# Performance work log

Hardware: AMD Instinct MI355X
Metric: run time of the kernel (lower is better)

The kernel has to match this reference:

```python
import jax, jax.numpy as jnp
import numpy as np

B, S, D = 1, 2048, 6144
H, KV, HD = 48, 8, 128  # query heads, kv heads, head dim
THETA = 10000.0


def _rope_tables(seq_len, head_dim, theta):
    pos = jnp.arange(seq_len, dtype=jnp.float32)
    inv_freq = 1.0 / (theta ** (jnp.arange(0, head_dim, 2, dtype=jnp.float32) / head_dim))
    freqs = pos[:, None] * inv_freq[None, :]                 # [S, HD/2]
    emb = jnp.concatenate([freqs, freqs], axis=-1)           # [S, HD]
    return jnp.cos(emb), jnp.sin(emb)


def setup_inputs() -> dict:
    key = jax.random.key(0)
    k1, k2, k3 = jax.random.split(key, 3)
    hidden_states = jax.random.normal(k1, (B, S, D), dtype=jnp.float32) * 0.02
    w_qkv = jax.random.normal(k2, (D, (H + 2 * KV) * HD), dtype=jnp.float32) * 0.02
    w_out = jax.random.normal(k3, (H * HD, D), dtype=jnp.float32) * 0.02
    cos, sin = _rope_tables(S, HD, THETA)
    return {"hidden_states": hidden_states, "cos": cos, "sin": sin,
            "w_qkv": w_qkv, "w_out": w_out}


def _rotate_half(x):
    x1, x2 = jnp.split(x, 2, axis=-1)
    return jnp.concatenate([-x2, x1], axis=-1)


def reference(hidden_states, cos, sin, w_qkv, w_out):
    b, s, d = hidden_states.shape
    # fused QKV projection
    qkv = jnp.einsum('bsd,de->bse', hidden_states, w_qkv)
    q = qkv[..., : H * HD].reshape(b, s, H, HD)
    k = qkv[..., H * HD: (H + KV) * HD].reshape(b, s, KV, HD)
    v = qkv[..., (H + KV) * HD:].reshape(b, s, KV, HD)
    # rotary embedding (rotate-half form)
    c = cos[None, :, None, :]
    sn = sin[None, :, None, :]
    q = q * c + _rotate_half(q) * sn
    k = k * c + _rotate_half(k) * sn
    # GQA: expand kv heads to query heads
    rep = H // KV
    k = jnp.repeat(k, rep, axis=2)  # [b, s, H, HD]
    v = jnp.repeat(v, rep, axis=2)
    scale = 1.0 / jnp.sqrt(jnp.float32(HD))
    scores = jnp.einsum('bqhd,bkhd->bhqk', q, k) * scale     # [b,H,S,S]
    causal = jnp.tril(jnp.ones((s, s), dtype=bool))
    scores = jnp.where(causal[None, None], scores, jnp.float32(-1e30))
    attn = jax.nn.softmax(scores, axis=-1)
    out = jnp.einsum('bhqk,bkhd->bqhd', attn, v).reshape(b, s, H * HD)
    return jnp.einsum('bsd,de->bse', out, w_out)
```

## Files before the change

kernel.cpp:

```cpp
#include <hip/hip_runtime.h>


#define S_   2048
#define D_   6144
#define H_   48
#define KV_  8
#define HD_  128
#define NQK  8192
#define REP  6

typedef __attribute__((ext_vector_type(8)))  __bf16 bf16x8;
typedef __attribute__((ext_vector_type(4)))  __bf16 bf16x4;
typedef __attribute__((ext_vector_type(2)))  __bf16 bf16x2;
typedef __attribute__((ext_vector_type(4)))  float  f32x4;
typedef __attribute__((ext_vector_type(16))) float  f32x16;
typedef __attribute__((ext_vector_type(4)))  float  float4v;

__device__ __forceinline__ void gl_lds16(const void* g, void* l) {
  __builtin_amdgcn_global_load_lds(
      (const __attribute__((address_space(1))) void*)g,
      (__attribute__((address_space(3))) void*)l, 16, 0, 0);
}

__device__ __forceinline__ unsigned pack2(float a, float b) {
  union { bf16x2 v; unsigned u; } x;
  x.v[0] = (__bf16)a; x.v[1] = (__bf16)b;
  return x.u;
}

__global__ __launch_bounds__(256) void cvt_bf16(const float* __restrict__ in,
                                                __bf16* __restrict__ out, int n4) {
  int stride = gridDim.x * 256;
  for (int i = blockIdx.x * 256 + threadIdx.x; i < n4; i += stride) {
    float4v v = ((const float4v*)in)[i];
    bf16x4 o;
    o[0] = (__bf16)v[0]; o[1] = (__bf16)v[1];
    o[2] = (__bf16)v[2]; o[3] = (__bf16)v[3];
    ((bf16x4*)out)[i] = o;
  }
}

__global__ __launch_bounds__(256) void wtrans(const float* __restrict__ src,
                                              __bf16* __restrict__ dst,
                                              int K, int N) {
  __shared__ float t[32][33];
  const int n0 = blockIdx.x * 32, k0 = blockIdx.y * 32;
  const int tx = threadIdx.x, ty = threadIdx.y;
#pragma unroll
  for (int r = 0; r < 4; ++r)
    t[ty + r * 8][tx] = src[(size_t)(k0 + ty + r * 8) * N + n0 + tx];
  __syncthreads();
#pragma unroll
  for (int r = 0; r < 4; ++r)
    dst[(size_t)(n0 + ty + r * 8) * K + k0 + tx] = (__bf16)t[tx][ty + r * 8];
}

__global__ __launch_bounds__(512, 2) void gemm_bt(const __bf16* __restrict__ A,
                                                  const __bf16* __restrict__ BT,
                                                  float* __restrict__ C,
                                                  int M, int N, int K) {
  __shared__ __align__(16) __bf16 As[2][256 * 64];
  __shared__ __align__(16) __bf16 Bs[2][256 * 64];
  const int tid = threadIdx.x;
  const int w = tid >> 6, l = tid & 63;
  const int lr = l & 15, lg = l >> 4;
  const int wm = w >> 2, wn = w & 3;
  const int nwg = gridDim.x * gridDim.y;
  int bid = blockIdx.y * gridDim.x + blockIdx.x;
  bid = (bid & 7) * (nwg >> 3) + (bid >> 3);
  const int m0 = (bid / gridDim.x) * 256, n0 = (bid % gridDim.x) * 256;
  const int nkt = K >> 6;

  auto stage_unit = [&](int T, int u) {
    const int buf = T & 1;
    const int k0 = T << 6;
    const __bf16* src = (u < 2) ? A : BT;
    const int base0 = (u < 2) ? m0 : n0;
    __bf16* dst = (u < 2) ? As[buf] : Bs[buf];
#pragma unroll
    for (int jj = 0; jj < 2; ++jj) {
      int j = (u & 1) * 2 + jj;
      int idx = j * 512 + tid;
      int row = idx >> 3;
      int c = (idx & 7) ^ (row & 7);
      gl_lds16(src + (size_t)(base0 + row) * K + k0 + c * 8,
               dst + (size_t)(j * 512 + w * 64) * 8);
    }
  };

  f32x4 acc[8][4] = {};
#pragma unroll
  for (int u = 0; u < 4; ++u) stage_unit(0, u);
  asm volatile("s_waitcnt vmcnt(0)" ::: "memory");
  __builtin_amdgcn_s_barrier();

  for (int T = 0; T < nkt; ++T) {
    const __bf16* Ab = As[T & 1];
    const __bf16* Bb = Bs[T & 1];
    bf16x8 bfr[4];
#pragma unroll
    for (int p = 0; p < 4; ++p) {
      const int kk = p >> 1, mh = p & 1;
      bf16x8 afr[4];
#pragma unroll
      for (int m = 0; m < 4; ++m) {
        int row = wm * 128 + (mh * 4 + m) * 16 + lr;
        afr[m] = *(const bf16x8*)(Ab + (size_t)row * 64
                                  + (((kk * 4 + lg) ^ (lr & 7)) * 8));
      }
      if (mh == 0) {
#pragma unroll
        for (int n = 0; n < 4; ++n) {
          int row = wn * 64 + n * 16 + lr;
          bfr[n] = *(const bf16x8*)(Bb + (size_t)row * 64
                                    + (((kk * 4 + lg) ^ (lr & 7)) * 8));
        }
      }
      if (p == 0 && T + 1 < nkt) {
#pragma unroll
        for (int u = 0; u < 4; ++u) stage_unit(T + 1, u);
      }
      if (p == 3 && T + 1 < nkt)
        asm volatile("s_waitcnt vmcnt(0)" ::: "memory");
      __builtin_amdgcn_s_barrier();
      asm volatile("s_waitcnt lgkmcnt(0)" ::: "memory");
      __builtin_amdgcn_sched_barrier(0);
      __builtin_amdgcn_s_setprio(1);
#pragma unroll
      for (int m = 0; m < 4; ++m)
#pragma unroll
        for (int n = 0; n < 4; ++n)
          acc[mh * 4 + m][n] = __builtin_amdgcn_mfma_f32_16x16x32_bf16(
              afr[m], bfr[n], acc[mh * 4 + m][n], 0, 0, 0);
      __builtin_amdgcn_s_setprio(0);
      __builtin_amdgcn_sched_barrier(0);
      __builtin_amdgcn_s_barrier();
    }
  }
#pragma unroll
  for (int m = 0; m < 8; ++m)
#pragma unroll
    for (int n = 0; n < 4; ++n)
#pragma unroll
      for (int j = 0; j < 4; ++j) {
        int row = m0 + wm * 128 + m * 16 + lg * 4 + j;
        int col = n0 + wn * 64 + n * 16 + lr;
        C[(size_t)row * N + col] = acc[m][n][j];
      }
}

__global__ __launch_bounds__(256) void rope_qk(const float* __restrict__ qkv,
                                               const float* __restrict__ cosT,
                                               const float* __restrict__ sinT,
                                               __bf16* __restrict__ Qo,
                                               __bf16* __restrict__ Ko) {
  const int s = blockIdx.x;
  const float* base = qkv + (size_t)s * NQK;
  const float* ct = cosT + s * HD_;
  const float* st = sinT + s * HD_;
  const float scale = 0.1275174313f;
  for (int idx = threadIdx.x; idx < H_ * HD_; idx += 256) {
    int h = idx >> 7, d = idx & 127;
    float x = base[idx];
    float r = (d < 64) ? -base[idx + 64] : base[idx - 64];
    Qo[((size_t)s * H_ + h) * HD_ + d] = (__bf16)((x * ct[d] + r * st[d]) * scale);
  }
  for (int idx = threadIdx.x; idx < KV_ * HD_; idx += 256) {
    int h = idx >> 7, d = idx & 127;
    float x = base[H_ * HD_ + idx];
    float r = (d < 64) ? -base[H_ * HD_ + idx + 64] : base[H_ * HD_ + idx - 64];
    Ko[((size_t)s * KV_ + h) * HD_ + d] = (__bf16)(x * ct[d] + r * st[d]);
  }
}

__global__ __launch_bounds__(256) void v_trans(const float* __restrict__ qkv,
                                               __bf16* __restrict__ Vt) {
  __shared__ float t[32][33];
  const int s0 = blockIdx.x * 32, d0 = blockIdx.y * 32, h = blockIdx.z;
  const int tx = threadIdx.x, ty = threadIdx.y;
#pragma unroll
  for (int r = 0; r < 4; ++r)
    t[ty + r * 8][tx] = qkv[(size_t)(s0 + ty + r * 8) * NQK + (H_ + KV_) * HD_ + h * HD_ + d0 + tx];
  __syncthreads();
#pragma unroll
  for (int r = 0; r < 4; ++r)
    Vt[((size_t)h * HD_ + d0 + ty + r * 8) * S_ + s0 + tx] = (__bf16)t[tx][ty + r * 8];
}

__global__ __launch_bounds__(256, 2) void attn(const __bf16* __restrict__ Q,
                                               const __bf16* __restrict__ Kb,
                                               const __bf16* __restrict__ Vt,
                                               __bf16* __restrict__ O) {
  __shared__ __align__(16) __bf16 Ks[2][64 * 128];
  __shared__ __align__(16) __bf16 Vs[2][128 * 64];
  const int bx = blockIdx.x, h = blockIdx.y, kvh = h / REP;
  const int tid = threadIdx.x, w = tid >> 6, l = tid & 63;
  const int c = l & 31, g = l >> 5;
  const int qb = bx * 128;
  const int qrow = qb + w * 32 + c;
  const int tmax_w = (qb + w * 32 + 31) >> 6;
  const int NT = (qb >> 6) + 2;

  auto stage = [&](int t) {
    const int buf = t & 1;
    const int kbase = t << 6;
#pragma unroll
    for (int j = 0; j < 4; ++j) {
      int idx = j * 256 + tid;
      int row = idx >> 4, cc = (idx & 15) ^ (row & 15);
      gl_lds16(Kb + ((size_t)(kbase + row) * KV_ + kvh) * HD_ + cc * 8,
               Ks[buf] + (size_t)(j * 256 + w * 64) * 8);
    }
#pragma unroll
    for (int j = 0; j < 4; ++j) {
      int idx = j * 256 + tid;
      int row = idx >> 3, cc = (idx & 7) ^ (row & 7);
      gl_lds16(Vt + (size_t)(kvh * HD_ + row) * S_ + kbase + cc * 8,
               Vs[buf] + (size_t)(j * 256 + w * 64) * 8);
    }
  };

  bf16x8 qf[8];
  const __bf16* qp = Q + ((size_t)qrow * H_ + h) * HD_ + g * 8;
#pragma unroll
  for (int st = 0; st < 8; ++st) qf[st] = *(const bf16x8*)(qp + st * 16);

  f32x16 o[4] = {};
  float m = -1e30f, lsum = 0.f;

  stage(0);
  __syncthreads();
  for (int t = 0; t < NT; ++t) {
    const int buf = t & 1;
    if (t + 1 < NT) stage(t + 1);
    if (t <= tmax_w) {
      const int kbase = t << 6;
      f32x16 s0 = {}, s1 = {};
      __builtin_amdgcn_s_setprio(1);
#pragma unroll
      for (int st = 0; st < 8; ++st) {
        int ch = ((st * 2 + g) ^ (c & 15)) * 8;
        bf16x8 k0 = *(const bf16x8*)(Ks[buf] + (size_t)c * 128 + ch);
        bf16x8 k1 = *(const bf16x8*)(Ks[buf] + (size_t)(32 + c) * 128 + ch);
        s0 = __builtin_amdgcn_mfma_f32_32x32x16_bf16(k0, qf[st], s0, 0, 0, 0);
        s1 = __builtin_amdgcn_mfma_f32_32x32x16_bf16(k1, qf[st], s1, 0, 0, 0);
      }
      __builtin_amdgcn_s_setprio(0);
      if (t == tmax_w) {
#pragma unroll
        for (int r = 0; r < 16; ++r) {
          int krow = (r & 3) + 8 * (r >> 2) + 4 * g;
          if (kbase + krow > qrow)      s0[r] = -1e30f;
          if (kbase + 32 + krow > qrow) s1[r] = -1e30f;
        }
      }
      float mj = s0[0];
#pragma unroll
      for (int r = 1; r < 16; ++r) mj = fmaxf(mj, s0[r]);
#pragma unroll
      for (int r = 0; r < 16; ++r) mj = fmaxf(mj, s1[r]);
      mj = fmaxf(mj, __shfl_xor(mj, 32));
      float mnew = fmaxf(m, mj);
      float sc = __builtin_amdgcn_exp2f(m - mnew);
      float rs = 0.f;
      float p0[16], p1[16];
#pragma unroll
      for (int r = 0; r < 16; ++r) { p0[r] = __builtin_amdgcn_exp2f(s0[r] - mnew); rs += p0[r]; }
#pragma unroll
      for (int r = 0; r < 16; ++r) { p1[r] = __builtin_amdgcn_exp2f(s1[r] - mnew); rs += p1[r]; }
      rs += __shfl_xor(rs, 32);
      lsum = lsum * sc + rs;
      m = mnew;
#pragma unroll
      for (int db = 0; db < 4; ++db)
#pragma unroll
        for (int r = 0; r < 16; ++r) o[db][r] *= sc;
      unsigned bq[4][4];
#pragma unroll
      for (int n = 0; n < 2; ++n)
#pragma unroll
        for (int tq = 0; tq < 2; ++tq) {
          const float* pp = n ? p1 : p0;
          unsigned q0 = pack2(pp[8 * tq + 0], pp[8 * tq + 1]);
          unsigned q1 = pack2(pp[8 * tq + 2], pp[8 * tq + 3]);
          unsigned q2 = pack2(pp[8 * tq + 4], pp[8 * tq + 5]);
          unsigned q3 = pack2(pp[8 * tq + 6], pp[8 * tq + 7]);
          unsigned v0 = g ? q0 : q2;
          unsigned v1 = g ? q1 : q3;
          unsigned sh0 = (unsigned)__shfl_xor((int)v0, 32);
          unsigned sh1 = (unsigned)__shfl_xor((int)v1, 32);
          int s = n * 2 + tq;
          bq[s][0] = g ? sh0 : q0;
          bq[s][1] = g ? sh1 : q1;
          bq[s][2] = g ? q2 : sh0;
          bq[s][3] = g ? q3 : sh1;
        }
      __builtin_amdgcn_s_setprio(1);
#pragma unroll
      for (int s = 0; s < 4; ++s) {
        union { unsigned u[4]; bf16x8 v; } bb;
        bb.u[0] = bq[s][0]; bb.u[1] = bq[s][1]; bb.u[2] = bq[s][2]; bb.u[3] = bq[s][3];
#pragma unroll
        for (int db = 0; db < 4; ++db) {
          int ch = ((s * 2 + g) ^ (c & 7)) * 8;
          bf16x8 vfr = *(const bf16x8*)(Vs[buf] + (size_t)(db * 32 + c) * 64 + ch);
          o[db] = __builtin_amdgcn_mfma_f32_32x32x16_bf16(vfr, bb.v, o[db], 0, 0, 0);
        }
      }
      __builtin_amdgcn_s_setprio(0);
    }
    if (t + 1 < NT) __syncthreads();
  }
  float inv = 1.f / lsum;
#pragma unroll
  for (int db = 0; db < 4; ++db)
#pragma unroll
    for (int rg = 0; rg < 4; ++rg) {
      bf16x4 ov;
#pragma unroll
      for (int j = 0; j < 4; ++j) ov[j] = (__bf16)(o[db][rg * 4 + j] * inv);
      *(bf16x4*)(O + (size_t)qrow * D_ + h * HD_ + db * 32 + rg * 8 + g * 4) = ov;
    }
}

extern "C" void kernel_launch(void* const* d_in, const int* in_sizes, int n_in,
                              void* d_out, int out_size, void* d_ws, size_t ws_size,
                              hipStream_t stream) {
  const float* hidden = (const float*)d_in[0];
  const float* cosT   = (const float*)d_in[1];
  const float* sinT   = (const float*)d_in[2];
  const float* w_qkv  = (const float*)d_in[3];
  const float* w_out  = (const float*)d_in[4];
  float* out = (float*)d_out;
  char* ws = (char*)d_ws;

  __bf16* wT  = (__bf16*)ws;
  __bf16* hb  = (__bf16*)(ws + 100663296);
  float*  qkv = (float*)(ws + 100663296 + 25165824);
  __bf16* q_b = (__bf16*)(ws + 100663296 + 25165824 + 67108864);
  __bf16* k_b = q_b + (size_t)S_ * H_ * HD_;
  __bf16* vt_b = k_b + (size_t)S_ * KV_ * HD_;

  cvt_bf16<<<dim3(2048), dim3(256), 0, stream>>>(hidden, hb, (int)((size_t)S_ * D_ / 4));
  wtrans<<<dim3(NQK / 32, D_ / 32), dim3(32, 8), 0, stream>>>(w_qkv, wT, D_, NQK);
  gemm_bt<<<dim3(NQK / 256, S_ / 256), dim3(512), 0, stream>>>(hb, wT, qkv, S_, NQK, D_);
  rope_qk<<<dim3(S_), dim3(256), 0, stream>>>(qkv, cosT, sinT, q_b, k_b);
  v_trans<<<dim3(S_ / 32, HD_ / 32, KV_), dim3(32, 8), 0, stream>>>(qkv, vt_b);
  wtrans<<<dim3(D_ / 32, D_ / 32), dim3(32, 8), 0, stream>>>(w_out, wT, D_, D_);
  attn<<<dim3(S_ / 128, H_), dim3(256), 0, stream>>>(q_b, k_b, vt_b, hb);
  gemm_bt<<<dim3(D_ / 256, S_ / 256), dim3(512), 0, stream>>>(hb, wT, out, S_, D_, D_);
}
```

Before: 713.0 us.

## Deepen GEMM LDS pipeline to four K=32 stages with three tiles in flight

Halves the GEMM K-tile from 64 to 32 and uses four LDS buffers, prefetching three tiles ahead instead of one. The vmcnt waits are changed from a full drain to partial waits, so global-to-LDS loads overlap more of the MFMA work. A new XOR swizzle suited to 32-wide rows is meant to avoid LDS bank conflicts. In exchange there are twice as many barriers per unit of K, and the waitcnt bookkeeping near the loop tail is more fragile.

```diff
diff --git a/kernel.cpp b/kernel.cpp
--- a/kernel.cpp
+++ b/kernel.cpp
@@ -59,8 +59,8 @@
                                                   const __bf16* __restrict__ BT,
                                                   float* __restrict__ C,
                                                   int M, int N, int K) {
-  __shared__ __align__(16) __bf16 As[2][256 * 64];
-  __shared__ __align__(16) __bf16 Bs[2][256 * 64];
+  __shared__ __align__(16) __bf16 As[4][256 * 32];
+  __shared__ __align__(16) __bf16 Bs[4][256 * 32];
   const int tid = threadIdx.x;
   const int w = tid >> 6, l = tid & 63;
   const int lr = l & 15, lg = l >> 4;
@@ -69,59 +69,52 @@
   int bid = blockIdx.y * gridDim.x + blockIdx.x;
   bid = (bid & 7) * (nwg >> 3) + (bid >> 3);
   const int m0 = (bid / gridDim.x) * 256, n0 = (bid % gridDim.x) * 256;
-  const int nkt = K >> 6;
-
-  auto stage_unit = [&](int T, int u) {
-    const int buf = T & 1;
-    const int k0 = T << 6;
-    const __bf16* src = (u < 2) ? A : BT;
-    const int base0 = (u < 2) ? m0 : n0;
-    __bf16* dst = (u < 2) ? As[buf] : Bs[buf];
-#pragma unroll
-    for (int jj = 0; jj < 2; ++jj) {
-      int j = (u & 1) * 2 + jj;
+  const int nkt = K >> 5;
+
+  auto stage = [&](int T) {
+    const int buf = T & 3;
+    const int k0 = T << 5;
+#pragma unroll
+    for (int j = 0; j < 2; ++j) {
       int idx = j * 512 + tid;
-      int row = idx >> 3;
-      int c = (idx & 7) ^ (row & 7);
-      gl_lds16(src + (size_t)(base0 + row) * K + k0 + c * 8,
-               dst + (size_t)(j * 512 + w * 64) * 8);
+      int row = idx >> 2;
+      int c = (idx & 3) ^ ((row ^ (row >> 2)) & 3);
+      gl_lds16(A  + (size_t)(m0 + row) * K + k0 + c * 8, As[buf] + (size_t)idx * 8);
+      gl_lds16(BT + (size_t)(n0 + row) * K + k0 + c * 8, Bs[buf] + (size_t)idx * 8);
     }
   };
 
   f32x4 acc[8][4] = {};
-#pragma unroll
-  for (int u = 0; u < 4; ++u) stage_unit(0, u);
-  asm volatile("s_waitcnt vmcnt(0)" ::: "memory");
+  stage(0); stage(1); stage(2);
+  asm volatile("s_waitcnt vmcnt(8)" ::: "memory");
   __builtin_amdgcn_s_barrier();
 
   for (int T = 0; T < nkt; ++T) {
-    const __bf16* Ab = As[T & 1];
-    const __bf16* Bb = Bs[T & 1];
+    const __bf16* Ab = As[T & 3];
+    const __bf16* Bb = Bs[T & 3];
     bf16x8 bfr[4];
 #pragma unroll
-    for (int p = 0; p < 4; ++p) {
-      const int kk = p >> 1, mh = p & 1;
+    for (int mh = 0; mh < 2; ++mh) {
       bf16x8 afr[4];
 #pragma unroll
       for (int m = 0; m < 4; ++m) {
         int row = wm * 128 + (mh * 4 + m) * 16 + lr;
-        afr[m] = *(const bf16x8*)(Ab + (size_t)row * 64
-                                  + (((kk * 4 + lg) ^ (lr & 7)) * 8));
+        afr[m] = *(const bf16x8*)(Ab + (size_t)row * 32
+                                  + (((lg ^ ((row ^ (row >> 2)) & 3))) * 8));
       }
       if (mh == 0) {
 #pragma unroll
         for (int n = 0; n < 4; ++n) {
           int row = wn * 64 + n * 16 + lr;
-          bfr[n] = *(const bf16x8*)(Bb + (size_t)row * 64
-                                    + (((kk * 4 + lg) ^ (lr & 7)) * 8));
+          bfr[n] = *(const bf16x8*)(Bb + (size_t)row * 32
+                                    + (((lg ^ ((row ^ (row >> 2)) & 3))) * 8));
         }
-      }
-      if (p == 0 && T + 1 < nkt) {
-#pragma unroll
-        for (int u = 0; u < 4; ++u) stage_unit(T + 1, u);
-      }
-      if (p == 3 && T + 1 < nkt)
-        asm volatile("s_waitcnt vmcnt(0)" ::: "memory");
+        if (T + 3 < nkt) stage(T + 3);
+      } else {
+        if (T + 4 <= nkt)      asm volatile("s_waitcnt vmcnt(8)" ::: "memory");
+        else if (T == nkt - 3) asm volatile("s_waitcnt vmcnt(4)" ::: "memory");
+        else if (T == nkt - 2) asm volatile("s_waitcnt vmcnt(0)" ::: "memory");
+      }
       __builtin_amdgcn_s_barrier();
       asm volatile("s_waitcnt lgkmcnt(0)" ::: "memory");
       __builtin_amdgcn_sched_barrier(0);
```

New measurement: 765.5 us. +7.4%, slower.

## Spread GEMM tile prefetch across k-phases and store QKV intermediate as bf16

Applied to the files above, without the earlier changes.

The GEMM main loop is restructured so the next k-tile's four staging units are issued one per MFMA phase, with a partial vmcnt wait, instead of all at once with a full drain. The aim is to overlap global-to-LDS copies with compute more evenly. The QKV projection now writes bf16 instead of fp32, which halves the intermediate traffic. rope_qk and v_trans are rewritten to read bf16 with vectorized accesses. Rounding the QKV output to bf16 before RoPE adds some precision loss, and the finer-grained waits risk reading LDS before the data has landed.

```diff
diff --git a/kernel.cpp b/kernel.cpp
--- a/kernel.cpp
+++ b/kernel.cpp
@@ -55,9 +55,10 @@
     dst[(size_t)(n0 + ty + r * 8) * K + k0 + tx] = (__bf16)t[tx][ty + r * 8];
 }
 
+template <typename CT>
 __global__ __launch_bounds__(512, 2) void gemm_bt(const __bf16* __restrict__ A,
                                                   const __bf16* __restrict__ BT,
-                                                  float* __restrict__ C,
+                                                  CT* __restrict__ C,
                                                   int M, int N, int K) {
   __shared__ __align__(16) __bf16 As[2][256 * 64];
   __shared__ __align__(16) __bf16 Bs[2][256 * 64];
@@ -87,55 +88,87 @@
                dst + (size_t)(j * 512 + w * 64) * 8);
     }
   };
+  auto rdA = [&](const __bf16* Ab, int mh, int kk, bf16x8* afr) {
+#pragma unroll
+    for (int m = 0; m < 4; ++m) {
+      int row = wm * 128 + (mh * 4 + m) * 16 + lr;
+      afr[m] = *(const bf16x8*)(Ab + (size_t)row * 64
+                                + (((kk * 4 + lg) ^ (lr & 7)) * 8));
+    }
+  };
+  auto rdB = [&](const __bf16* Bb, int kk, bf16x8* bfr) {
+#pragma unroll
+    for (int n = 0; n < 4; ++n) {
+      int row = wn * 64 + n * 16 + lr;
+      bfr[n] = *(const bf16x8*)(Bb + (size_t)row * 64
+                                + (((kk * 4 + lg) ^ (lr & 7)) * 8));
+    }
+  };
 
   f32x4 acc[8][4] = {};
 #pragma unroll
   for (int u = 0; u < 4; ++u) stage_unit(0, u);
-  asm volatile("s_waitcnt vmcnt(0)" ::: "memory");
-  __builtin_amdgcn_s_barrier();
 
   for (int T = 0; T < nkt; ++T) {
     const __bf16* Ab = As[T & 1];
     const __bf16* Bb = Bs[T & 1];
-    bf16x8 bfr[4];
-#pragma unroll
-    for (int p = 0; p < 4; ++p) {
-      const int kk = p >> 1, mh = p & 1;
-      bf16x8 afr[4];
-#pragma unroll
-      for (int m = 0; m < 4; ++m) {
-        int row = wm * 128 + (mh * 4 + m) * 16 + lr;
-        afr[m] = *(const bf16x8*)(Ab + (size_t)row * 64
-                                  + (((kk * 4 + lg) ^ (lr & 7)) * 8));
-      }
-      if (mh == 0) {
-#pragma unroll
-        for (int n = 0; n < 4; ++n) {
-          int row = wn * 64 + n * 16 + lr;
-          bfr[n] = *(const bf16x8*)(Bb + (size_t)row * 64
-                                    + (((kk * 4 + lg) ^ (lr & 7)) * 8));
-        }
-      }
-      if (p == 0 && T + 1 < nkt) {
-#pragma unroll
-        for (int u = 0; u < 4; ++u) stage_unit(T + 1, u);
-      }
-      if (p == 3 && T + 1 < nkt)
-        asm volatile("s_waitcnt vmcnt(0)" ::: "memory");
-      __builtin_amdgcn_s_barrier();
-      asm volatile("s_waitcnt lgkmcnt(0)" ::: "memory");
-      __builtin_amdgcn_sched_barrier(0);
-      __builtin_amdgcn_s_setprio(1);
-#pragma unroll
-      for (int m = 0; m < 4; ++m)
-#pragma unroll
-        for (int n = 0; n < 4; ++n)
-          acc[mh * 4 + m][n] = __builtin_amdgcn_mfma_f32_16x16x32_bf16(
-              afr[m], bfr[n], acc[mh * 4 + m][n], 0, 0, 0);
-      __builtin_amdgcn_s_setprio(0);
-      __builtin_amdgcn_sched_barrier(0);
-      __builtin_amdgcn_s_barrier();
-    }
+    bf16x8 afr[4], bfr[4];
+    if (T + 1 < nkt) {
+      stage_unit(T + 1, 0);
+      asm volatile("s_waitcnt vmcnt(2)" ::: "memory");
+    } else {
+      asm volatile("s_waitcnt vmcnt(0)" ::: "memory");
+    }
+    __builtin_amdgcn_s_barrier();
+    rdA(Ab, 0, 0, afr);
+    rdB(Bb, 0, bfr);
+    asm volatile("s_waitcnt lgkmcnt(0)" ::: "memory");
+    __builtin_amdgcn_sched_barrier(0);
+    __builtin_amdgcn_s_setprio(1);
+#pragma unroll
+    for (int m = 0; m < 4; ++m)
+#pragma unroll
+      for (int n = 0; n < 4; ++n)
+        acc[m][n] = __builtin_amdgcn_mfma_f32_16x16x32_bf16(afr[m], bfr[n], acc[m][n], 0, 0, 0);
+    __builtin_amdgcn_s_setprio(0);
+    rdA(Ab, 1, 0, afr);
+    if (T + 1 < nkt) stage_unit(T + 1, 1);
+    __builtin_amdgcn_s_barrier();
+    asm volatile("s_waitcnt lgkmcnt(0)" ::: "memory");
+    __builtin_amdgcn_sched_barrier(0);
+    __builtin_amdgcn_s_setprio(1);
+#pragma unroll
+    for (int m = 0; m < 4; ++m)
+#pragma unroll
+      for (int n = 0; n < 4; ++n)
+        acc[4 + m][n] = __builtin_amdgcn_mfma_f32_16x16x32_bf16(afr[m], bfr[n], acc[4 + m][n], 0, 0, 0);
+    __builtin_amdgcn_s_setprio(0);
+    rdA(Ab, 0, 1, afr);
+    rdB(Bb, 1, bfr);
+    if (T + 1 < nkt) stage_unit(T + 1, 2);
+    __builtin_amdgcn_s_barrier();
+    asm volatile("s_waitcnt lgkmcnt(0)" ::: "memory");
+    __builtin_amdgcn_sched_barrier(0);
+    __builtin_amdgcn_s_setprio(1);
+#pragma unroll
+    for (int m = 0; m < 4; ++m)
+#pragma unroll
+      for (int n = 0; n < 4; ++n)
+        acc[m][n] = __builtin_amdgcn_mfma_f32_16x16x32_bf16(afr[m], bfr[n], acc[m][n], 0, 0, 0);
+    __builtin_amdgcn_s_setprio(0);
+    rdA(Ab, 1, 1, afr);
+    if (T + 1 < nkt) stage_unit(T + 1, 3);
+    __builtin_amdgcn_s_barrier();
+    asm volatile("s_waitcnt lgkmcnt(0)" ::: "memory");
+    __builtin_amdgcn_sched_barrier(0);
+    __builtin_amdgcn_s_setprio(1);
+#pragma unroll
+    for (int m = 0; m < 4; ++m)
+#pragma unroll
+      for (int n = 0; n < 4; ++n)
+        acc[4 + m][n] = __builtin_amdgcn_mfma_f32_16x16x32_bf16(afr[m], bfr[n], acc[4 + m][n], 0, 0, 0);
+    __builtin_amdgcn_s_setprio(0);
+    __builtin_amdgcn_s_barrier();
   }
 #pragma unroll
   for (int m = 0; m < 8; ++m)
@@ -145,46 +178,65 @@
       for (int j = 0; j < 4; ++j) {
         int row = m0 + wm * 128 + m * 16 + lg * 4 + j;
         int col = n0 + wn * 64 + n * 16 + lr;
-        C[(size_t)row * N + col] = acc[m][n][j];
+        C[(size_t)row * N + col] = (CT)acc[m][n][j];
       }
 }
 
-__global__ __launch_bounds__(256) void rope_qk(const float* __restrict__ qkv,
+__global__ __launch_bounds__(256) void rope_qk(const __bf16* __restrict__ qkv,
                                                const float* __restrict__ cosT,
                                                const float* __restrict__ sinT,
                                                __bf16* __restrict__ Qo,
                                                __bf16* __restrict__ Ko) {
   const int s = blockIdx.x;
-  const float* base = qkv + (size_t)s * NQK;
+  const __bf16* base = qkv + (size_t)s * NQK;
   const float* ct = cosT + s * HD_;
   const float* st = sinT + s * HD_;
   const float scale = 0.1275174313f;
-  for (int idx = threadIdx.x; idx < H_ * HD_; idx += 256) {
-    int h = idx >> 7, d = idx & 127;
-    float x = base[idx];
-    float r = (d < 64) ? -base[idx + 64] : base[idx - 64];
-    Qo[((size_t)s * H_ + h) * HD_ + d] = (__bf16)((x * ct[d] + r * st[d]) * scale);
+  for (int q4 = threadIdx.x; q4 < H_ * HD_ / 4; q4 += 256) {
+    int h = q4 >> 5, d = (q4 & 31) * 4;
+    bf16x4 x  = *(const bf16x4*)(base + h * HD_ + d);
+    bf16x4 xr = (d < 64) ? *(const bf16x4*)(base + h * HD_ + d + 64)
+                         : *(const bf16x4*)(base + h * HD_ + d - 64);
+    float4v c4 = *(const float4v*)(ct + d);
+    float4v s4 = *(const float4v*)(st + d);
+    bf16x4 o;
+#pragma unroll
+    for (int j = 0; j < 4; ++j) {
+      float r = (d < 64) ? -(float)xr[j] : (float)xr[j];
+      o[j] = (__bf16)(((float)x[j] * c4[j] + r * s4[j]) * scale);
+    }
+    *(bf16x4*)(Qo + ((size_t)s * H_ + h) * HD_ + d) = o;
   }
-  for (int idx = threadIdx.x; idx < KV_ * HD_; idx += 256) {
-    int h = idx >> 7, d = idx & 127;
-    float x = base[H_ * HD_ + idx];
-    float r = (d < 64) ? -base[H_ * HD_ + idx + 64] : base[H_ * HD_ + idx - 64];
-    Ko[((size_t)s * KV_ + h) * HD_ + d] = (__bf16)(x * ct[d] + r * st[d]);
+  for (int q4 = threadIdx.x; q4 < KV_ * HD_ / 4; q4 += 256) {
+    int h = q4 >> 5, d = (q4 & 31) * 4;
+    const __bf16* kb = base + H_ * HD_;
+    bf16x4 x  = *(const bf16x4*)(kb + h * HD_ + d);
+    bf16x4 xr = (d < 64) ? *(const bf16x4*)(kb + h * HD_ + d + 64)
+                         : *(const bf16x4*)(kb + h * HD_ + d - 64);
+    float4v c4 = *(const float4v*)(ct + d);
+    float4v s4 = *(const float4v*)(st + d);
+    bf16x4 o;
+#pragma unroll
+    for (int j = 0; j < 4; ++j) {
+      float r = (d < 64) ? -(float)xr[j] : (float)xr[j];
+      o[j] = (__bf16)((float)x[j] * c4[j] + r * s4[j]);
+    }
+    *(bf16x4*)(Ko + ((size_t)s * KV_ + h) * HD_ + d) = o;
   }
 }
 
-__global__ __launch_bounds__(256) void v_trans(const float* __restrict__ qkv,
+__global__ __launch_bounds__(256) void v_trans(const __bf16* __restrict__ qkv,
                                                __bf16* __restrict__ Vt) {
-  __shared__ float t[32][33];
+  __shared__ __bf16 t[32][36];
   const int s0 = blockIdx.x * 32, d0 = blockIdx.y * 32, h = blockIdx.z;
   const int tx = threadIdx.x, ty = threadIdx.y;
-#pragma unroll
-  for (int r = 0; r < 4; ++r)
-    t[ty + r * 8][tx] = qkv[(size_t)(s0 + ty + r * 8) * NQK + (H_ + KV_) * HD_ + h * HD_ + d0 + tx];
+  *(bf16x4*)&t[ty][tx * 4] =
+      *(const bf16x4*)(qkv + (size_t)(s0 + ty) * NQK + (H_ + KV_) * HD_ + h * HD_ + d0 + tx * 4);
   __syncthreads();
-#pragma unroll
-  for (int r = 0; r < 4; ++r)
-    Vt[((size_t)h * HD_ + d0 + ty + r * 8) * S_ + s0 + tx] = (__bf16)t[tx][ty + r * 8];
+  bf16x4 o;
+#pragma unroll
+  for (int j = 0; j < 4; ++j) o[j] = t[tx * 4 + j][ty];
+  *(bf16x4*)(Vt + ((size_t)h * HD_ + d0 + ty) * S_ + s0 + tx * 4) = o;
 }
 
 __global__ __launch_bounds__(256, 2) void attn(const __bf16* __restrict__ Q,
@@ -334,19 +386,19 @@
   float* out = (float*)d_out;
   char* ws = (char*)d_ws;
 
-  __bf16* wT  = (__bf16*)ws;
-  __bf16* hb  = (__bf16*)(ws + 100663296);
-  float*  qkv = (float*)(ws + 100663296 + 25165824);
-  __bf16* q_b = (__bf16*)(ws + 100663296 + 25165824 + 67108864);
-  __bf16* k_b = q_b + (size_t)S_ * H_ * HD_;
+  __bf16* wT   = (__bf16*)ws;
+  __bf16* hb   = (__bf16*)(ws + 100663296);
+  __bf16* qkvb = (__bf16*)(ws + 100663296 + 25165824);
+  __bf16* q_b  = (__bf16*)(ws + 100663296 + 25165824 + 33554432);
+  __bf16* k_b  = q_b + (size_t)S_ * H_ * HD_;
   __bf16* vt_b = k_b + (size_t)S_ * KV_ * HD_;
 
   cvt_bf16<<<dim3(2048), dim3(256), 0, stream>>>(hidden, hb, (int)((size_t)S_ * D_ / 4));
   wtrans<<<dim3(NQK / 32, D_ / 32), dim3(32, 8), 0, stream>>>(w_qkv, wT, D_, NQK);
-  gemm_bt<<<dim3(NQK / 256, S_ / 256), dim3(512), 0, stream>>>(hb, wT, qkv, S_, NQK, D_);
-  rope_qk<<<dim3(S_), dim3(256), 0, stream>>>(qkv, cosT, sinT, q_b, k_b);
-  v_trans<<<dim3(S_ / 32, HD_ / 32, KV_), dim3(32, 8), 0, stream>>>(qkv, vt_b);
+  gemm_bt<__bf16><<<dim3(NQK / 256, S_ / 256), dim3(512), 0, stream>>>(hb, wT, qkvb, S_, NQK, D_);
+  rope_qk<<<dim3(S_), dim3(256), 0, stream>>>(qkvb, cosT, sinT, q_b, k_b);
+  v_trans<<<dim3(S_ / 32, HD_ / 32, KV_), dim3(8, 32), 0, stream>>>(qkvb, vt_b);
   wtrans<<<dim3(D_ / 32, D_ / 32), dim3(32, 8), 0, stream>>>(w_out, wT, D_, D_);
   attn<<<dim3(S_ / 128, H_), dim3(256), 0, stream>>>(q_b, k_b, vt_b, hb);
-  gemm_bt<<<dim3(D_ / 256, S_ / 256), dim3(512), 0, stream>>>(hb, wT, out, S_, D_, D_);
-}
+  gemm_bt<float><<<dim3(D_ / 256, S_ / 256), dim3(512), 0, stream>>>(hb, wT, out, S_, D_, D_);
+}
```

Result: faster. 686.1 us (-3.8%).
